# Kernel optimization log

Hardware: AMD Instinct MI355X
Metric: run time of the kernel (lower is better)

The kernel has to match this reference:

```python
import jax, jax.numpy as jnp
import numpy as np

DAMPENING = 0.3          # dampening_factor
REC_DAMPENING = 0.4      # recurrent_dampening_factor
DT = 1.0
MAX_DELAY = 5
N_BASIS = 5


@jax.custom_vjp
def spike_function(v_scaled):
    # hard threshold with triangular pseudo-derivative (custom gradient)
    return (v_scaled > 0.0).astype(v_scaled.dtype)

def _spike_fwd(v_scaled):
    return spike_function(v_scaled), v_scaled

def _spike_bwd(v_scaled, g):
    return (g * DAMPENING * jnp.maximum(1.0 - jnp.abs(v_scaled), 0.0),)

spike_function.defvjp(_spike_fwd, _spike_bwd)


def setup_inputs() -> dict:
    key = jax.random.key(0)
    ks = jax.random.split(key, 12)
    N, E, T, B = 50000, 2_000_000, 40, 1
    D, n5 = MAX_DELAY, N * N_BASIS
    inp = {}
    inp['weights'] = jax.random.normal(ks[0], (E,), jnp.float32) * 0.01
    inp['edge_basis'] = jax.random.uniform(ks[1], (E, N_BASIS), jnp.float32)
    inp['ext_input'] = jax.random.normal(ks[2], (B, T, n5), jnp.float32) * 0.02
    inp['decay'] = 0.9 + 0.09 * jax.random.uniform(ks[3], (N,), jnp.float32)
    inp['current_factor'] = jax.random.uniform(ks[4], (N,), jnp.float32)
    inp['gathered_g'] = jax.random.normal(ks[5], (N,), jnp.float32) * 0.01
    inp['v_th'] = jnp.ones((N,), jnp.float32)          # normalized threshold
    inp['v_reset'] = jnp.zeros((N,), jnp.float32)
    inp['normalizer'] = jnp.ones((N,), jnp.float32)    # v_th - e_l
    inp['t_ref'] = 2.0 * jnp.ones((N,), jnp.float32)
    inp['exp_dt_k'] = 0.8 + 0.19 * jax.random.uniform(ks[6], (N, 2), jnp.float32)
    inp['asc_amps'] = jax.random.normal(ks[7], (N, 2), jnp.float32) * 0.01
    inp['syn_decay'] = jax.random.uniform(ks[8], (n5,), jnp.float32)
    inp['psc_initial'] = jax.random.uniform(ks[9], (n5,), jnp.float32)
    inp['pre_idx'] = jax.random.randint(ks[10], (E,), 0, D * N, jnp.int32)
    inp['post_idx'] = jax.random.randint(ks[11], (E,), 0, N, jnp.int32)
    return inp


def reference(weights, edge_basis, ext_input, decay, current_factor, gathered_g,
              v_th, v_reset, normalizer, t_ref, exp_dt_k, asc_amps,
              syn_decay, psc_initial, pre_idx, post_idx):
    B, T, n5 = ext_input.shape
    N = n5 // N_BASIS
    D = MAX_DELAY
    # per-edge weight across the 5 synaptic basis filters: [E,5]
    ew = weights[:, None] * edge_basis

    def rec_input(z_flat):  # z_flat: [B, D*N] delayed spike buffer (flattened)
        zg = jnp.take(z_flat, pre_idx, axis=1)                # [B,E] gather presynaptic spikes
        contrib = zg[:, :, None] * ew[None]                    # [B,E,5]
        out = jax.vmap(lambda c: jax.ops.segment_sum(c, post_idx, num_segments=N))(contrib)
        return out.reshape(B, N * N_BASIS)                     # [B,N*5]

    def step(carry, x_t):
        v, r, asc, psc, z_buf = carry
        # recurrent dampening: scale gradient through recurrent spikes
        zd = z_buf * REC_DAMPENING
        zb = jax.lax.stop_gradient(z_buf - zd) + zd
        i_rec = rec_input(zb.reshape(B, D * N))
        new_psc = psc * syn_decay + (i_rec + x_t) * psc_initial      # [B,N*5]
        input_current = new_psc.reshape(B, N, N_BASIS).sum(-1)       # [B,N]
        prev_z = z_buf[:, 0]                                         # most recent spikes
        new_asc = exp_dt_k * asc + prev_z[:, :, None] * asc_amps     # [B,N,2]
        c1 = input_current + new_asc.sum(-1) + gathered_g
        new_v = decay * v + current_factor * c1
        new_v = jnp.where(prev_z > 0.5, v_reset, new_v)              # hard reset
        v_sc = (new_v - v_th) / normalizer
        z = spike_function(v_sc)
        z = jnp.where(r > 0.0, jnp.zeros_like(z), z)                 # refractory block
        new_r = jnp.maximum(r + z * t_ref - DT, 0.0)
        new_buf = jnp.concatenate([z[:, None], z_buf[:, :-1]], axis=1)
        return (new_v, new_r, new_asc, new_psc, new_buf), z

    v0 = jnp.broadcast_to(v_reset, (B, N)).astype(jnp.float32)
    r0 = jnp.zeros((B, N), jnp.float32)
    asc0 = jnp.zeros((B, N, 2), jnp.float32)
    psc0 = jnp.zeros((B, n5), jnp.float32)
    buf0 = jnp.zeros((B, D, N), jnp.float32)
    x_seq = jnp.transpose(ext_input, (1, 0, 2))  # [T,B,N*5]
    _, z_seq = jax.lax.scan(step, (v0, r0, asc0, psc0, buf0), x_seq)
    return jnp.transpose(z_seq, (1, 0, 2))  # [B,T,N] spikes
```

## Files before the change

### kernel.cpp

```cpp
#include <hip/hip_runtime.h>

#define NB_ 5
#define MD_ 5
#define CSL 128
#define CAP 6144
#define CH2 8192
#define RING 6


__global__ __launch_bounds__(256) void partition_kernel(
    const int* __restrict__ pre_idx,
    int* __restrict__ gcur,
    unsigned* __restrict__ part,
    int E, int N)
{
    __shared__ unsigned srt[CH2];
    __shared__ unsigned short bkt[CH2];
    __shared__ int hist[512];
    __shared__ int lbase[512];
    __shared__ int pos[512];
    __shared__ int gbase[512];
    __shared__ int tmp[256];

    const int t  = threadIdx.x;
    const int e0 = blockIdx.x * CH2;
    const int cnt = min(CH2, E - e0);

    hist[t] = 0; hist[t + 256] = 0;
    __syncthreads();

    for (int i = t; i < cnt; i += 256) {
        int pre = pre_idx[e0 + i];
        int d = pre / N;
        int n = pre - d * N;
        atomicAdd(&hist[n >> 7], 1);
    }
    __syncthreads();

    int a = hist[2 * t], b = hist[2 * t + 1], s = a + b;
    tmp[t] = s;
    __syncthreads();
    int x = s;
    for (int off = 1; off < 256; off <<= 1) {
        int y = (t >= off) ? tmp[t - off] : 0;
        __syncthreads();
        x += y;
        tmp[t] = x;
        __syncthreads();
    }
    int ep = x - s;
    lbase[2 * t] = ep;         pos[2 * t] = ep;
    lbase[2 * t + 1] = ep + a; pos[2 * t + 1] = ep + a;
    gbase[2 * t]     = a ? atomicAdd(&gcur[2 * t], a) : 0;
    gbase[2 * t + 1] = b ? atomicAdd(&gcur[2 * t + 1], b) : 0;
    __syncthreads();

    for (int i = t; i < cnt; i += 256) {
        int pre = pre_idx[e0 + i];
        int d = pre / N;
        int n = pre - d * N;
        int bk = n >> 7;
        int p = atomicAdd(&pos[bk], 1);
        srt[p] = ((unsigned)(n & (CSL - 1)) << 24) | ((unsigned)d << 21)
               | (unsigned)(e0 + i);
        bkt[p] = (unsigned short)bk;
    }
    __syncthreads();

    for (int j = t; j < cnt; j += 256) {
        int bk = bkt[j];
        int off2 = gbase[bk] + (j - lbase[bk]);
        if (off2 < CAP)
            part[(size_t)bk * CAP + off2] = srt[j];
    }
}

__global__ __launch_bounds__(256) void bucket_sort_kernel(
    const int* __restrict__ gcur,
    const unsigned* __restrict__ part,
    unsigned* __restrict__ edgeRec,
    uint2* __restrict__ rp,
    const float* __restrict__ decay, const float* __restrict__ cf,
    const float* __restrict__ g,     const float* __restrict__ vth,
    const float* __restrict__ vrst,  const float* __restrict__ nrm,
    const float* __restrict__ tref,  const float* __restrict__ ek,
    const float* __restrict__ am,
    float4* __restrict__ pk, float* __restrict__ v,
    int N)
{
    __shared__ int h[CSL];
    __shared__ int sc_[CSL];
    __shared__ int pos_[CSL];
    int c = blockIdx.x, t = threadIdx.x;

    if (t < CSL) {
        int n = c * CSL + t;
        if (n < N) {
            pk[3 * n]     = make_float4(decay[n], cf[n], g[n], vth[n]);
            pk[3 * n + 1] = make_float4(vrst[n], nrm[n], tref[n], ek[2 * n]);
            pk[3 * n + 2] = make_float4(ek[2 * n + 1], am[2 * n], am[2 * n + 1], 0.0f);
            v[n] = vrst[n];
        }
    }

    int cnt = min(gcur[c], CAP);
    size_t base = (size_t)c * CAP;
    if (t < CSL) h[t] = 0;
    __syncthreads();
    for (int i = t; i < cnt; i += 256)
        atomicAdd(&h[part[base + i] >> 24], 1);
    __syncthreads();
    if (t < CSL) sc_[t] = h[t];
    __syncthreads();
    for (int off = 1; off < CSL; off <<= 1) {
        int y = 0;
        if (t < CSL && t >= off) y = sc_[t - off];
        __syncthreads();
        if (t < CSL && t >= off) sc_[t] += y;
        __syncthreads();
    }
    if (t < CSL) {
        int end = sc_[t];
        pos_[t] = (int)base + end - h[t];
        int gn = c * CSL + t;
        if (gn < N)
            rp[gn] = make_uint2((unsigned)(base + end - h[t]),
                                (unsigned)(base + end));
    }
    __syncthreads();
    for (int i = t; i < cnt; i += 256) {
        unsigned q = part[base + i];
        int dst = atomicAdd(&pos_[q >> 24], 1);
        edgeRec[dst] = q;
    }
}


__global__ __launch_bounds__(256) void step_kernel(
    const float* __restrict__ x_t,
    float*       __restrict__ psc,
    const float* __restrict__ sd,
    const float* __restrict__ pi,
    const float4* __restrict__ pk,
    float* __restrict__ v,
    float* __restrict__ r,
    float* __restrict__ asc,
    float* __restrict__ ring,
    const int* __restrict__ scnt,
    int*       __restrict__ scnt_new,
    const float* __restrict__ out_prev,
    float*       __restrict__ out_t,
    const uint2*    __restrict__ rp,
    const unsigned* __restrict__ edgeRec,
    const float*    __restrict__ weights,
    const float*    __restrict__ edge_basis,
    const int*      __restrict__ post_idx,
    int t, int n5, int N)
{
    __shared__ int   nf_s;
    __shared__ uint2 rowsL[256];
    __shared__ int   scL[256];
    __shared__ int   pref[257];

    const int tloc = threadIdx.x;
    const int n = blockIdx.x * blockDim.x + tloc;
    const bool has = (n < N);
    if (tloc == 0) nf_s = 0;
    __syncthreads();

    const int* sw = scnt + t;
    int scw = sw[0] + sw[1] + sw[2] + sw[3] + sw[4];

    float z = 0.0f;
    if (has) {
        float ir0 = 0.f, ir1 = 0.f, ir2 = 0.f, ir3 = 0.f, ir4 = 0.f;
        float* rg = ring + (size_t)(t % RING) * n5 + (size_t)n * NB_;
        if (scw > 0) {
            ir0 = rg[0]; ir1 = rg[1]; ir2 = rg[2]; ir3 = rg[3]; ir4 = rg[4];
            rg[0] = 0.f; rg[1] = 0.f; rg[2] = 0.f; rg[3] = 0.f; rg[4] = 0.f;
        }

        const float* xp  = x_t + (size_t)n * NB_;
        float*       pp  = psc + (size_t)n * NB_;
        const float* sdp = sd  + (size_t)n * NB_;
        const float* pip = pi  + (size_t)n * NB_;
        float ic = 0.0f, pv;
        pv = pp[0] * sdp[0] + (ir0 + xp[0]) * pip[0]; pp[0] = pv; ic += pv;
        pv = pp[1] * sdp[1] + (ir1 + xp[1]) * pip[1]; pp[1] = pv; ic += pv;
        pv = pp[2] * sdp[2] + (ir2 + xp[2]) * pip[2]; pp[2] = pv; ic += pv;
        pv = pp[3] * sdp[3] + (ir3 + xp[3]) * pip[3]; pp[3] = pv; ic += pv;
        pv = pp[4] * sdp[4] + (ir4 + xp[4]) * pip[4]; pp[4] = pv; ic += pv;

        float4 P0 = pk[3 * n], P1 = pk[3 * n + 1], P2 = pk[3 * n + 2];

        float pz = (t > 0) ? out_prev[n] : 0.0f;

        float a0 = P1.w * asc[2 * n]     + pz * P2.y;
        float a1 = P2.x * asc[2 * n + 1] + pz * P2.z;
        asc[2 * n]     = a0;
        asc[2 * n + 1] = a1;

        float c1 = ic + (a0 + a1) + P0.z;
        float nv = P0.x * v[n] + P0.y * c1;
        if (pz > 0.5f) nv = P1.x;

        float vsc = (nv - P0.w) / P1.y;
        z = (vsc > 0.0f) ? 1.0f : 0.0f;
        float rr = r[n];
        if (rr > 0.0f) z = 0.0f;

        r[n] = fmaxf(rr + z * P1.z - 1.0f, 0.0f);
        v[n] = nv;
        out_t[n] = z;

        if (z != 0.0f) {
            int idx = atomicAdd(&nf_s, 1);
            rowsL[idx] = rp[n];
        }
    }

    unsigned long long m = __ballot(z != 0.0f);
    if ((tloc & 63) == 0 && m)
        atomicAdd(scnt_new, (int)__popcll(m));

    __syncthreads();
    int nf = nf_s;
    if (nf == 0) return;

    int cnt = (tloc < nf) ? (int)(rowsL[tloc].y - rowsL[tloc].x) : 0;
    scL[tloc] = cnt;
    __syncthreads();
    int x = cnt;
    for (int off = 1; off < 256; off <<= 1) {
        int y = (tloc >= off) ? scL[tloc - off] : 0;
        __syncthreads();
        x += y;
        scL[tloc] = x;
        __syncthreads();
    }
    pref[tloc + 1] = scL[tloc];
    if (tloc == 0) pref[0] = 0;
    __syncthreads();

    int tot = pref[nf];
    for (int j = tloc; j < tot; j += 256) {
        int lo = 0, hi = nf - 1;
        while (lo < hi) {
            int mid = (lo + hi + 1) >> 1;
            if (pref[mid] <= j) lo = mid; else hi = mid - 1;
        }
        int i = (int)rowsL[lo].x + (j - pref[lo]);
        unsigned q = edgeRec[i];
        int d = (int)((q >> 21) & 7u);
        int e = (int)(q & 0x1FFFFFu);
        float w = weights[e];
        const float* bs = edge_basis + (size_t)e * NB_;
        float* dst = ring + (size_t)((t + 1 + d) % RING) * n5
                   + (size_t)post_idx[e] * NB_;
        atomicAdd(dst + 0, w * bs[0]);
        atomicAdd(dst + 1, w * bs[1]);
        atomicAdd(dst + 2, w * bs[2]);
        atomicAdd(dst + 3, w * bs[3]);
        atomicAdd(dst + 4, w * bs[4]);
    }
}


extern "C" void kernel_launch(void* const* d_in, const int* in_sizes, int n_in,
                              void* d_out, int out_size, void* d_ws, size_t ws_size,
                              hipStream_t stream)
{
    const float* weights        = (const float*)d_in[0];
    const float* edge_basis     = (const float*)d_in[1];
    const float* ext_input      = (const float*)d_in[2];
    const float* decay          = (const float*)d_in[3];
    const float* current_factor = (const float*)d_in[4];
    const float* gathered_g     = (const float*)d_in[5];
    const float* v_th           = (const float*)d_in[6];
    const float* v_reset        = (const float*)d_in[7];
    const float* normalizer     = (const float*)d_in[8];
    const float* t_ref          = (const float*)d_in[9];
    const float* exp_dt_k       = (const float*)d_in[10];
    const float* asc_amps       = (const float*)d_in[11];
    const float* syn_decay      = (const float*)d_in[12];
    const float* psc_initial    = (const float*)d_in[13];
    const int*   pre_idx        = (const int*)d_in[14];
    const int*   post_idx       = (const int*)d_in[15];

    const int E  = in_sizes[0];
    const int N  = in_sizes[3];
    const int n5 = N * NB_;
    const int T  = in_sizes[2] / n5;

    const int NC = (N + CSL - 1) / CSL;

    float* out = (float*)d_out;

    char* wsb = (char*)d_ws;
    size_t o = 0;
    int*   gcur = (int*)(wsb + o);   o += 512 * 4;
    int*   scnt = (int*)(wsb + o);   o += (size_t)(T + MD_) * 4;
    o = (o + 15) & ~(size_t)15;
    float* psc  = (float*)(wsb + o); o += (size_t)n5 * 4;
    float* r    = (float*)(wsb + o); o += (size_t)N * 4;
    float* asc  = (float*)(wsb + o); o += (size_t)2 * N * 4;
    o = (o + 15) & ~(size_t)15;
    float* ring = (float*)(wsb + o); o += (size_t)RING * n5 * 4;
    size_t zero_bytes = o;
    float*  v       = (float*)(wsb + o);  o += (size_t)N * 4;
    float4* pk      = (float4*)(wsb + o); o += (size_t)N * 12 * 4;
    uint2*  rp      = (uint2*)(wsb + o);  o += (size_t)N * 8;
    o = (o + 15) & ~(size_t)15;
    unsigned* part    = (unsigned*)(wsb + o); o += (size_t)NC * CAP * 4;
    unsigned* edgeRec = (unsigned*)(wsb + o); o += (size_t)NC * CAP * 4;

    hipMemsetAsync(d_ws, 0, zero_bytes, stream);

    const int nbe = (E + CH2 - 1) / CH2;
    partition_kernel<<<nbe, 256, 0, stream>>>(pre_idx, gcur, part, E, N);
    bucket_sort_kernel<<<NC, 256, 0, stream>>>(
        gcur, part, edgeRec, rp,
        decay, current_factor, gathered_g, v_th, v_reset, normalizer, t_ref,
        exp_dt_k, asc_amps, pk, v, N);

    const int nblk = (N + 255) / 256;
    for (int t = 0; t < T; ++t) {
        step_kernel<<<nblk, 256, 0, stream>>>(
            ext_input + (size_t)t * n5,
            psc, syn_decay, psc_initial,
            pk, v, r, asc,
            ring, scnt, scnt + MD_ + t,
            out + (size_t)(t > 0 ? t - 1 : 0) * N,
            out + (size_t)t * N,
            rp, edgeRec, weights, edge_basis, post_idx,
            t, n5, N);
    }
}
```

Measured before the change: 275.2 us.

## Replace block-wide scan edge scatter with per-wavefront ballot loop

Each wavefront now ballots its spiking neurons and walks their edge rows one at a time, with all 64 lanes striding through each row. This replaces the block-level shared-memory list, the prefix scan with many __syncthreads and the binary-search mapping. The aim is to cut barrier and scan overhead per timestep, at the cost of poorer lane use when rows are short or uneven. The partition chunk size CH2 is also halved, which changes the shared-memory footprint and chunking of the one-time partition kernel.

```diff
diff --git a/kernel.cpp b/kernel.cpp
--- a/kernel.cpp
+++ b/kernel.cpp
@@ -4,7 +4,7 @@
 #define MD_ 5
 #define CSL 128
 #define CAP 6144
-#define CH2 8192
+#define CH2 4096
 #define RING 6
 
 
@@ -157,16 +157,10 @@
     const int*      __restrict__ post_idx,
     int t, int n5, int N)
 {
-    __shared__ int   nf_s;
-    __shared__ uint2 rowsL[256];
-    __shared__ int   scL[256];
-    __shared__ int   pref[257];
-
     const int tloc = threadIdx.x;
     const int n = blockIdx.x * blockDim.x + tloc;
     const bool has = (n < N);
-    if (tloc == 0) nf_s = 0;
-    __syncthreads();
+    const int lane = tloc & 63;
 
     const int* sw = scnt + t;
     int scw = sw[0] + sw[1] + sw[2] + sw[3] + sw[4];
@@ -212,56 +206,37 @@
         r[n] = fmaxf(rr + z * P1.z - 1.0f, 0.0f);
         v[n] = nv;
         out_t[n] = z;
-
-        if (z != 0.0f) {
-            int idx = atomicAdd(&nf_s, 1);
-            rowsL[idx] = rp[n];
+    }
+
+    unsigned long long fm = __ballot(z != 0.0f);
+    if (lane == 0 && fm)
+        atomicAdd(scnt_new, (int)__popcll(fm));
+
+    if (fm) {
+        unsigned rs0 = 0, re0 = 0;
+        if (z != 0.0f) { uint2 row = rp[n]; rs0 = row.x; re0 = row.y; }
+
+        unsigned long long fm2 = fm;
+        while (fm2) {
+            int src = (int)(__ffsll((long long)fm2) - 1);
+            fm2 &= fm2 - 1;
+            unsigned rs = __shfl(rs0, src);
+            unsigned re = __shfl(re0, src);
+            for (unsigned i = rs + lane; i < re; i += 64) {
+                unsigned q = edgeRec[i];
+                int d = (int)((q >> 21) & 7u);
+                int e = (int)(q & 0x1FFFFFu);
+                float w = weights[e];
+                const float* bs = edge_basis + (size_t)e * NB_;
+                float* dst = ring + (size_t)((t + 1 + d) % RING) * n5
+                           + (size_t)post_idx[e] * NB_;
+                atomicAdd(dst + 0, w * bs[0]);
+                atomicAdd(dst + 1, w * bs[1]);
+                atomicAdd(dst + 2, w * bs[2]);
+                atomicAdd(dst + 3, w * bs[3]);
+                atomicAdd(dst + 4, w * bs[4]);
+            }
         }
-    }
-
-    unsigned long long m = __ballot(z != 0.0f);
-    if ((tloc & 63) == 0 && m)
-        atomicAdd(scnt_new, (int)__popcll(m));
-
-    __syncthreads();
-    int nf = nf_s;
-    if (nf == 0) return;
-
-    int cnt = (tloc < nf) ? (int)(rowsL[tloc].y - rowsL[tloc].x) : 0;
-    scL[tloc] = cnt;
-    __syncthreads();
-    int x = cnt;
-    for (int off = 1; off < 256; off <<= 1) {
-        int y = (tloc >= off) ? scL[tloc - off] : 0;
-        __syncthreads();
-        x += y;
-        scL[tloc] = x;
-        __syncthreads();
-    }
-    pref[tloc + 1] = scL[tloc];
-    if (tloc == 0) pref[0] = 0;
-    __syncthreads();
-
-    int tot = pref[nf];
-    for (int j = tloc; j < tot; j += 256) {
-        int lo = 0, hi = nf - 1;
-        while (lo < hi) {
-            int mid = (lo + hi + 1) >> 1;
-            if (pref[mid] <= j) lo = mid; else hi = mid - 1;
-        }
-        int i = (int)rowsL[lo].x + (j - pref[lo]);
-        unsigned q = edgeRec[i];
-        int d = (int)((q >> 21) & 7u);
-        int e = (int)(q & 0x1FFFFFu);
-        float w = weights[e];
-        const float* bs = edge_basis + (size_t)e * NB_;
-        float* dst = ring + (size_t)((t + 1 + d) % RING) * n5
-                   + (size_t)post_idx[e] * NB_;
-        atomicAdd(dst + 0, w * bs[0]);
-        atomicAdd(dst + 1, w * bs[1]);
-        atomicAdd(dst + 2, w * bs[2]);
-        atomicAdd(dst + 3, w * bs[3]);
-        atomicAdd(dst + 4, w * bs[4]);
     }
 }
 
```

Result: faster. 251.5 us (-8.6%).
